# Kernel tuning notes

Hardware: AMD Instinct MI355X
Metric: run time of the kernel (lower is better)

The kernel has to match this reference:

```python
import jax, jax.numpy as jnp
import numpy as np

F = 845   # feature_num
P = 39    # field_num
K = 32    # implicit_vector_dim
B = 32768 # batch


def _field_ids():
    # feature_to_field(n) = n if n < 13 else (n - 13) // K + 13
    n = np.arange(F)
    return np.where(n < 13, n, (n - 13) // K + 13).astype(np.int32)


def setup_inputs() -> dict:
    key = jax.random.key(0)
    k0, k1, k2, k3 = jax.random.split(key, 4)
    # scale inputs/params down so the quadratic term does not saturate sigmoid
    X = jax.random.normal(k0, (B, F), jnp.float32) * 0.05
    field_matrix = jax.random.normal(k1, (F, P, K), jnp.float32) * 0.1
    a = jax.random.normal(k2, (F, F), jnp.float32)
    w_lin = jax.random.normal(k3, (F, 1), jnp.float32) * 0.02
    b_lin = jnp.zeros((1,), jnp.float32)
    return {"X": X, "field_matrix": field_matrix, "a": a,
            "w_lin": w_lin, "b_lin": b_lin}


def reference(X, field_matrix, a, w_lin, b_lin):
    # The original loop computes, per feature i:
    #   result[b] += X[b, i] * sum_j a[i, j] * X[b, j]
    #                * <field_matrix[i, field(i)], field_matrix[j, field(j)]>
    # i.e. a batched quadratic form X W X^T (diagonal) with
    #   W[i, j] = a[i, j] * (V @ V.T)[i, j],  V[i] = field_matrix[i, field(i)].
    fid = jnp.asarray(_field_ids())
    V = field_matrix[jnp.arange(F), fid]        # [F, K] own-field vectors
    W = a * (V @ V.T)                           # [F, F]
    quad = jnp.sum((X @ W) * X, axis=-1)        # [B]
    lin = X @ w_lin[:, 0] + b_lin[0]            # [B]
    # original casts to double at the end; we stay in float32 (math identical)
    return jax.nn.sigmoid(lin + quad)
```

## Files before the change

kernel.cpp:

```cpp
#include <hip/hip_runtime.h>
#include <hip/hip_bf16.h>
#include <math.h>

typedef unsigned short ushort_t;
typedef unsigned int   uint_t;

typedef __attribute__((ext_vector_type(8))) __bf16 bf16x8;
typedef __attribute__((ext_vector_type(4))) float  f32x4;

#define BATCH 32768
#define FDIM  845
#define FP    896
#define NBLK  7
#define MSTR  128

#define PREP_BLKS 196
#define CONV_BLKS 27040
#define PAD_BLKS  8192

__device__ __forceinline__ int fld(int n) { return (n < 13) ? n : (((n - 13) >> 5) + 13); }

__device__ __forceinline__ ushort_t f2bf(float f) {
    uint_t u = __builtin_bit_cast(uint_t, f);
    uint_t r = u + 0x7FFFu + ((u >> 16) & 1u);
    return (ushort_t)(r >> 16);
}
__device__ __forceinline__ float bf2f(ushort_t h) {
    uint_t u = ((uint_t)h) << 16;
    return __builtin_bit_cast(float, u);
}

__device__ __forceinline__ void gload_lds16(const ushort_t* g, ushort_t* l) {
    __builtin_amdgcn_global_load_lds(
        (const __attribute__((address_space(1))) void*)g,
        (__attribute__((address_space(3))) void*)l, 16, 0, 0);
}

__global__ __launch_bounds__(256, 2)
void prep_all(const float* __restrict__ X, const float* __restrict__ fm,
              const float* __restrict__ a, const float* __restrict__ wl,
              ushort_t* __restrict__ Xb, ushort_t* __restrict__ WbT) {
    __shared__ float    As[64 * 65];
    __shared__ float    At[64 * 65];
    __shared__ ushort_t Vi[64 * 32];
    __shared__ ushort_t Vj[64 * 32];

    const int tid = threadIdx.x;
    const int bx  = blockIdx.x;

    if (bx >= PREP_BLKS) {
        const int cb = bx - PREP_BLKS;
        if (cb < CONV_BLKS) {
            const uint_t e0 = ((uint_t)cb * 256 + tid) * 4;
            const float4 x = *(const float4*)(X + e0);
            const uint_t row0 = e0 / 845u;
            const uint_t col0 = e0 - row0 * 845u;
            const float xv[4] = {x.x, x.y, x.z, x.w};
            #pragma unroll
            for (int j = 0; j < 4; ++j) {
                const uint_t row = row0 + ((col0 + j >= 845u) ? 1u : 0u);
                Xb[(size_t)(e0 + j) + 51u * row] = f2bf(xv[j]);
            }
        } else {
            const uint_t p   = (uint_t)(cb - CONV_BLKS) * 256 + tid;
            const uint_t row = p >> 6, q = p & 63;
            if (q < 51) Xb[(size_t)row * FP + FDIM + q] = (q == 0) ? (ushort_t)0x3F80 : (ushort_t)0;
        }
        return;
    }

    const int i0 = (bx % 14) * 64, j0 = (bx / 14) * 64;
    const int ib128 = i0 >> 7, jb128 = j0 >> 7;
    if (ib128 > jb128) return;
    const bool offd = (ib128 < jb128);
    const int wave = tid >> 6, lane = tid & 63;
    const int l15  = lane & 15, l4 = lane >> 4;

    {
        const int row = tid >> 2;
        const int kq  = (tid & 3) * 8;
        union { ushort_t u[8]; uint4 v; } pi, pj;
        const int gi = i0 + row, gj = j0 + row;
        #pragma unroll
        for (int q = 0; q < 8; ++q) {
            float vi = 0.0f, vj = 0.0f;
            if (gi < FDIM) vi = fm[(size_t)(gi * 39 + fld(gi)) * 32 + kq + q];
            if (gj < FDIM) vj = fm[(size_t)(gj * 39 + fld(gj)) * 32 + kq + q];
            pi.u[q] = f2bf(vi);
            pj.u[q] = f2bf(vj);
        }
        *(uint4*)&Vi[row * 32 + kq] = pi.v;
        *(uint4*)&Vj[row * 32 + kq] = pj.v;
    }
    {
        const int row = tid >> 2, seg = tid & 3;
        const int gi  = i0 + row, gj2 = j0 + row;
        #pragma unroll
        for (int q = 0; q < 16; ++q) {
            const int cl = seg * 16 + q;
            const int gj = j0 + cl;
            As[row * 65 + cl] = (gi < FDIM && gj < FDIM) ? a[(size_t)gi * FDIM + gj] : 0.0f;
            if (offd) {
                const int gi2 = i0 + cl;
                At[row * 65 + cl] = (gj2 < FDIM && gi2 < FDIM) ? a[(size_t)gj2 * FDIM + gi2] : 0.0f;
            }
        }
    }
    __syncthreads();

    bf16x8 af = *(const bf16x8*)&Vj[(wave * 16 + l15) * 32 + l4 * 8];
    f32x4 acc[4];
    #pragma unroll
    for (int it = 0; it < 4; ++it) {
        bf16x8 bf = *(const bf16x8*)&Vi[(it * 16 + l15) * 32 + l4 * 8];
        acc[it] = __builtin_amdgcn_mfma_f32_16x16x32_bf16(af, bf, (f32x4){0.f,0.f,0.f,0.f}, 0, 0, 0);
    }

    #pragma unroll
    for (int it = 0; it < 4; ++it) {
        #pragma unroll
        for (int r = 0; r < 4; ++r) {
            const int jl = wave * 16 + l4 * 4 + r;
            const int il = it * 16 + l15;
            const int gi = i0 + il, gj = j0 + jl;
            float aij = As[il * 65 + jl];
            if (offd) aij += At[jl * 65 + il];
            float w = acc[it][r] * aij;
            if (gj == FDIM) w = (gi < FDIM) ? wl[gi] : 0.0f;
            WbT[(size_t)gj * FP + gi] = f2bf(w);
        }
    }
}

__global__ __launch_bounds__(256, 2)
void ffm_gemm(const ushort_t* __restrict__ Xb, const ushort_t* __restrict__ WbT,
              float* __restrict__ qpart) {
    __shared__ ushort_t As[256 * 64];
    __shared__ ushort_t Bs[128 * 64];

    const int tid  = threadIdx.x;
    const int wave = tid >> 6, lane = tid & 63;
    const int l15  = lane & 15, l4 = lane >> 4;

    const int bid  = blockIdx.x;
    const int xcd  = bid & 7;
    const int slot = bid >> 3;
    const int nb   = 6 - (slot % 7);
    const int m0   = (xcd * 16 + slot / 7) * 256;
    const int n0   = nb * 128;

    const int r8 = lane >> 3;
    const int s8 = lane & 7;

    f32x4 acc[4][8];
    #pragma unroll
    for (int i = 0; i < 4; ++i)
        #pragma unroll
        for (int j = 0; j < 8; ++j) acc[i][j] = (f32x4){0.f, 0.f, 0.f, 0.f};

    const int kimax = (nb + 1) * 2;
    for (int kt = 0; kt < kimax; ++kt) {
        const int k0 = kt * 64;
        __syncthreads();
        #pragma unroll
        for (int h = 0; h < 8; ++h) {
            const int row = wave * 64 + h * 8 + r8;
            const int sg  = s8 ^ (row & 7);
            gload_lds16(Xb + (size_t)(m0 + row) * FP + k0 + sg * 8,
                        &As[(wave * 64 + h * 8) * 64]);
        }
        #pragma unroll
        for (int h = 0; h < 4; ++h) {
            const int row = wave * 32 + h * 8 + r8;
            const int sg  = s8 ^ (row & 7);
            gload_lds16(WbT + (size_t)(n0 + row) * FP + k0 + sg * 8,
                        &Bs[(wave * 32 + h * 8) * 64]);
        }
        __syncthreads();

        bf16x8 af[4][2];
        #pragma unroll
        for (int i = 0; i < 4; ++i) {
            const int r = wave * 64 + i * 16 + l15;
            #pragma unroll
            for (int h = 0; h < 2; ++h) {
                const int s = (h * 4 + l4) ^ (r & 7);
                af[i][h] = *(const bf16x8*)&As[r * 64 + s * 8];
            }
        }
        #pragma unroll
        for (int j = 0; j < 8; ++j) {
            const int r = j * 16 + l15;
            const int s0 = l4 ^ (r & 7);
            const int s1 = (4 + l4) ^ (r & 7);
            const bf16x8 b0 = *(const bf16x8*)&Bs[r * 64 + s0 * 8];
            const bf16x8 b1 = *(const bf16x8*)&Bs[r * 64 + s1 * 8];
            #pragma unroll
            for (int i = 0; i < 4; ++i) {
                acc[i][j] = __builtin_amdgcn_mfma_f32_16x16x32_bf16(af[i][0], b0, acc[i][j], 0, 0, 0);
                acc[i][j] = __builtin_amdgcn_mfma_f32_16x16x32_bf16(af[i][1], b1, acc[i][j], 0, 0, 0);
            }
        }
    }

    float q[4][4] = {};
    #pragma unroll
    for (int i = 0; i < 4; ++i)
        #pragma unroll
        for (int j = 0; j < 8; ++j) {
            const int col = n0 + j * 16 + l15;
            #pragma unroll
            for (int r = 0; r < 4; ++r) {
                const int row = m0 + wave * 64 + i * 16 + l4 * 4 + r;
                q[i][r] += acc[i][j][r] * bf2f(Xb[(size_t)row * FP + col]);
            }
        }
    #pragma unroll
    for (int off = 1; off < 16; off <<= 1)
        #pragma unroll
        for (int i = 0; i < 4; ++i)
            #pragma unroll
            for (int r = 0; r < 4; ++r) q[i][r] += __shfl_xor(q[i][r], off, 64);

    if (l15 == 0) {
        float* dst = qpart + (size_t)nb * BATCH;
        #pragma unroll
        for (int i = 0; i < 4; ++i)
            #pragma unroll
            for (int r = 0; r < 4; ++r)
                dst[m0 + wave * 64 + i * 16 + l4 * 4 + r] = q[i][r];
    }
}

__global__ void finish(const float* __restrict__ qpart, const float* __restrict__ blin,
                       float* __restrict__ out) {
    int b = blockIdx.x * 256 + threadIdx.x;
    float s = blin[0];
    #pragma unroll
    for (int p = 0; p < 7; ++p) s += qpart[(size_t)p * BATCH + b];
    out[b] = 1.0f / (1.0f + expf(-s));
}

extern "C" void kernel_launch(void* const* d_in, const int* in_sizes, int n_in,
                              void* d_out, int out_size, void* d_ws, size_t ws_size,
                              hipStream_t stream) {
    const float* X  = (const float*)d_in[0];
    const float* fm = (const float*)d_in[1];
    const float* a  = (const float*)d_in[2];
    const float* wl = (const float*)d_in[3];
    const float* bl = (const float*)d_in[4];
    float* out = (float*)d_out;

    char* ws = (char*)d_ws;
    ushort_t* Xb    = (ushort_t*)ws;
    ushort_t* WbT   = (ushort_t*)(ws + 58720256);
    float*    qpart = (float*)   (ws + 60325888);

    prep_all<<<PREP_BLKS + CONV_BLKS + PAD_BLKS, 256, 0, stream>>>(X, fm, a, wl, Xb, WbT);
    ffm_gemm<<<MSTR * NBLK,        256, 0, stream>>>(Xb, WbT, qpart);
    finish  <<<BATCH / 256,        256, 0, stream>>>(qpart, bl, out);
}
```

Before: 228.0 us.

## Prepack W into MFMA fragment layout and load B straight to registers

The prep kernel now writes the weight matrix in a chunked layout that matches the MFMA B-operand fragment, so each lane reads its 16-byte fragment directly from global memory instead of staging B through LDS. The GEMM M-tile is halved from 256 to 128 rows, doubling the block count, shrinking accumulators and LDS, and raising the occupancy hint to 3. This removes B's LDS traffic and the B LDS reads, but each block now reloads B from global/L2 directly, and per-block reuse of B drops with the smaller M tile.

```diff
diff --git a/kernel.cpp b/kernel.cpp
--- a/kernel.cpp
+++ b/kernel.cpp
@@ -12,7 +12,8 @@
 #define FDIM  845
 #define FP    896
 #define NBLK  7
-#define MSTR  128
+#define MBLK  256
+#define KCHK  28
 
 #define PREP_BLKS 196
 #define CONV_BLKS 27040
@@ -39,7 +40,7 @@
 __global__ __launch_bounds__(256, 2)
 void prep_all(const float* __restrict__ X, const float* __restrict__ fm,
               const float* __restrict__ a, const float* __restrict__ wl,
-              ushort_t* __restrict__ Xb, ushort_t* __restrict__ WbT) {
+              ushort_t* __restrict__ Xb, ushort_t* __restrict__ Bp) {
     __shared__ float    As[64 * 65];
     __shared__ float    At[64 * 65];
     __shared__ ushort_t Vi[64 * 32];
@@ -127,16 +128,17 @@
             if (offd) aij += At[jl * 65 + il];
             float w = acc[it][r] * aij;
             if (gj == FDIM) w = (gi < FDIM) ? wl[gi] : 0.0f;
-            WbT[(size_t)gj * FP + gi] = f2bf(w);
-        }
-    }
-}
-
-__global__ __launch_bounds__(256, 2)
-void ffm_gemm(const ushort_t* __restrict__ Xb, const ushort_t* __restrict__ WbT,
+            const int chunk = (gj >> 4) * KCHK + (gi >> 5);
+            const int lin   = ((gi >> 3) & 3) * 16 + (gj & 15);
+            Bp[(size_t)chunk * 512 + lin * 8 + (gi & 7)] = f2bf(w);
+        }
+    }
+}
+
+__global__ __launch_bounds__(256, 3)
+void ffm_gemm(const ushort_t* __restrict__ Xb, const ushort_t* __restrict__ Bp,
               float* __restrict__ qpart) {
-    __shared__ ushort_t As[256 * 64];
-    __shared__ ushort_t Bs[128 * 64];
+    __shared__ ushort_t As[128 * 64];
 
     const int tid  = threadIdx.x;
     const int wave = tid >> 6, lane = tid & 63;
@@ -146,89 +148,84 @@
     const int xcd  = bid & 7;
     const int slot = bid >> 3;
     const int nb   = 6 - (slot % 7);
-    const int m0   = (xcd * 16 + slot / 7) * 256;
+    const int m0   = (xcd * 32 + slot / 7) * 128;
     const int n0   = nb * 128;
 
     const int r8 = lane >> 3;
     const int s8 = lane & 7;
 
-    f32x4 acc[4][8];
-    #pragma unroll
-    for (int i = 0; i < 4; ++i)
+    f32x4 acc[2][8];
+    #pragma unroll
+    for (int i = 0; i < 2; ++i)
         #pragma unroll
         for (int j = 0; j < 8; ++j) acc[i][j] = (f32x4){0.f, 0.f, 0.f, 0.f};
+
+    const ushort_t* bbase = Bp + (size_t)(nb * 8) * KCHK * 512 + lane * 8;
 
     const int kimax = (nb + 1) * 2;
     for (int kt = 0; kt < kimax; ++kt) {
         const int k0 = kt * 64;
         __syncthreads();
         #pragma unroll
-        for (int h = 0; h < 8; ++h) {
-            const int row = wave * 64 + h * 8 + r8;
-            const int sg  = s8 ^ (row & 7);
-            gload_lds16(Xb + (size_t)(m0 + row) * FP + k0 + sg * 8,
-                        &As[(wave * 64 + h * 8) * 64]);
-        }
-        #pragma unroll
         for (int h = 0; h < 4; ++h) {
             const int row = wave * 32 + h * 8 + r8;
             const int sg  = s8 ^ (row & 7);
-            gload_lds16(WbT + (size_t)(n0 + row) * FP + k0 + sg * 8,
-                        &Bs[(wave * 32 + h * 8) * 64]);
-        }
+            gload_lds16(Xb + (size_t)(m0 + row) * FP + k0 + sg * 8,
+                        &As[(wave * 32 + h * 8) * 64]);
+        }
+        bf16x8 bfv[8][2];
+        #pragma unroll
+        for (int j = 0; j < 8; ++j)
+            #pragma unroll
+            for (int h = 0; h < 2; ++h)
+                bfv[j][h] = *(const bf16x8*)(bbase + (size_t)(j * KCHK + kt * 2 + h) * 512);
         __syncthreads();
 
-        bf16x8 af[4][2];
-        #pragma unroll
-        for (int i = 0; i < 4; ++i) {
-            const int r = wave * 64 + i * 16 + l15;
+        bf16x8 afr[2][2];
+        #pragma unroll
+        for (int i = 0; i < 2; ++i) {
+            const int r = wave * 32 + i * 16 + l15;
             #pragma unroll
             for (int h = 0; h < 2; ++h) {
                 const int s = (h * 4 + l4) ^ (r & 7);
-                af[i][h] = *(const bf16x8*)&As[r * 64 + s * 8];
-            }
-        }
-        #pragma unroll
-        for (int j = 0; j < 8; ++j) {
-            const int r = j * 16 + l15;
-            const int s0 = l4 ^ (r & 7);
-            const int s1 = (4 + l4) ^ (r & 7);
-            const bf16x8 b0 = *(const bf16x8*)&Bs[r * 64 + s0 * 8];
-            const bf16x8 b1 = *(const bf16x8*)&Bs[r * 64 + s1 * 8];
-            #pragma unroll
-            for (int i = 0; i < 4; ++i) {
-                acc[i][j] = __builtin_amdgcn_mfma_f32_16x16x32_bf16(af[i][0], b0, acc[i][j], 0, 0, 0);
-                acc[i][j] = __builtin_amdgcn_mfma_f32_16x16x32_bf16(af[i][1], b1, acc[i][j], 0, 0, 0);
-            }
-        }
-    }
-
-    float q[4][4] = {};
-    #pragma unroll
-    for (int i = 0; i < 4; ++i)
+                afr[i][h] = *(const bf16x8*)&As[r * 64 + s * 8];
+            }
+        }
+        #pragma unroll
+        for (int j = 0; j < 8; ++j)
+            #pragma unroll
+            for (int i = 0; i < 2; ++i) {
+                acc[i][j] = __builtin_amdgcn_mfma_f32_16x16x32_bf16(afr[i][0], bfv[j][0], acc[i][j], 0, 0, 0);
+                acc[i][j] = __builtin_amdgcn_mfma_f32_16x16x32_bf16(afr[i][1], bfv[j][1], acc[i][j], 0, 0, 0);
+            }
+    }
+
+    float q[2][4] = {};
+    #pragma unroll
+    for (int i = 0; i < 2; ++i)
         #pragma unroll
         for (int j = 0; j < 8; ++j) {
             const int col = n0 + j * 16 + l15;
             #pragma unroll
             for (int r = 0; r < 4; ++r) {
-                const int row = m0 + wave * 64 + i * 16 + l4 * 4 + r;
+                const int row = m0 + wave * 32 + i * 16 + l4 * 4 + r;
                 q[i][r] += acc[i][j][r] * bf2f(Xb[(size_t)row * FP + col]);
             }
         }
     #pragma unroll
     for (int off = 1; off < 16; off <<= 1)
         #pragma unroll
-        for (int i = 0; i < 4; ++i)
+        for (int i = 0; i < 2; ++i)
             #pragma unroll
             for (int r = 0; r < 4; ++r) q[i][r] += __shfl_xor(q[i][r], off, 64);
 
     if (l15 == 0) {
         float* dst = qpart + (size_t)nb * BATCH;
         #pragma unroll
-        for (int i = 0; i < 4; ++i)
+        for (int i = 0; i < 2; ++i)
             #pragma unroll
             for (int r = 0; r < 4; ++r)
-                dst[m0 + wave * 64 + i * 16 + l4 * 4 + r] = q[i][r];
+                dst[m0 + wave * 32 + i * 16 + l4 * 4 + r] = q[i][r];
     }
 }
 
@@ -253,10 +250,10 @@
 
     char* ws = (char*)d_ws;
     ushort_t* Xb    = (ushort_t*)ws;
-    ushort_t* WbT   = (ushort_t*)(ws + 58720256);
+    ushort_t* Bp    = (ushort_t*)(ws + 58720256);
     float*    qpart = (float*)   (ws + 60325888);
 
-    prep_all<<<PREP_BLKS + CONV_BLKS + PAD_BLKS, 256, 0, stream>>>(X, fm, a, wl, Xb, WbT);
-    ffm_gemm<<<MSTR * NBLK,        256, 0, stream>>>(Xb, WbT, qpart);
+    prep_all<<<PREP_BLKS + CONV_BLKS + PAD_BLKS, 256, 0, stream>>>(X, fm, a, wl, Xb, Bp);
+    ffm_gemm<<<MBLK * NBLK,        256, 0, stream>>>(Xb, Bp, qpart);
     finish  <<<BATCH / 256,        256, 0, stream>>>(qpart, bl, out);
 }
```

Result: slower. 235.4 us (+3.2%).
